# Kernel tuning notes

Measured on AMD Instinct MI355X. Metric: run time of the kernel, lower is better.

The kernel has to match this reference:

```python
import jax, jax.numpy as jnp
import numpy as np

DIM = 1024
HEADS = 16
HD = DIM // HEADS            # 64
MLP = 4 * DIM                # 4096
IN_OUT = MLP + 3 * DIM       # 7168, in_proj out dim
OUT_IN = MLP + DIM           # 5120, out_proj in dim
OUT_OUT = 2 * DIM            # 2048, out_proj out dim
R = 2                        # residual PQ levels
K = 64                       # codebook size
NCB = HEADS                  # num_codebooks = num_heads * codebooks_ratio
IN_CLUSTERS = HEADS * (IN_OUT // DIM)                 # 112
OUT_CLUSTERS = HEADS * max(1, OUT_OUT // OUT_IN)      # 16
SUB_IN = DIM // NCB          # 64
SUB_OUT = OUT_IN // NCB      # 320
EPS = 1e-5


def setup_inputs() -> dict:
    key = jax.random.key(0)
    k1, k2, k3, k4, k5 = jax.random.split(key, 5)
    B, N = 4, 1024
    x = jax.random.normal(k1, (B, N, DIM), jnp.float32)
    in_codebooks = jax.random.normal(k2, (R, IN_CLUSTERS, NCB, K, SUB_IN), jnp.float32) * 0.02
    in_indices = jax.random.randint(k3, (R, IN_OUT, NCB), 0, K, jnp.int32)
    out_codebooks = jax.random.normal(k4, (R, OUT_CLUSTERS, NCB, K, SUB_OUT), jnp.float32) * 0.02
    out_indices = jax.random.randint(k5, (R, OUT_OUT, NCB), 0, K, jnp.int32)
    return {"x": x, "in_codebooks": in_codebooks, "in_indices": in_indices,
            "out_codebooks": out_codebooks, "out_indices": out_indices}


def _decode_weight(cb, idx):
    """Decode RPQ weight. cb: (R, n_clusters, n_codebooks, K, sub), idx: (R, O, n_codebooks).
    Returns dense weight (O, n_codebooks*sub)."""
    Rr, nclust, C, _, sub = cb.shape
    O = idx.shape[1]
    cluster = jnp.arange(O) // (O // nclust)                       # per-row cluster id
    w = cb[jnp.arange(Rr)[:, None, None],
           cluster[None, :, None],
           jnp.arange(C)[None, None, :],
           idx]                                                    # (R, O, C, sub)
    return w.sum(0).reshape(O, C * sub)


def reference(x, in_codebooks, in_indices, out_codebooks, out_indices):
    B, N, C = x.shape
    res = x
    # LayerNorm without affine
    mu = x.mean(-1, keepdims=True)
    var = x.var(-1, keepdims=True)
    xn = (x - mu) * jax.lax.rsqrt(var + EPS)
    # in_proj: dequant + GEMM
    Win = _decode_weight(in_codebooks, in_indices)                 # (IN_OUT, DIM)
    h = jnp.einsum('bnc,oc->bno', xn, Win)                         # (B, N, IN_OUT)
    xm, q, k, v = jnp.split(h, [MLP, MLP + DIM, MLP + 2 * DIM], axis=-1)
    q = q.reshape(B, N, HEADS, HD).transpose(0, 2, 1, 3)
    k = k.reshape(B, N, HEADS, HD).transpose(0, 2, 1, 3)
    v = v.reshape(B, N, HEADS, HD).transpose(0, 2, 1, 3)
    scale = HD ** -0.5
    attn = jax.nn.softmax(jnp.einsum('bhqd,bhkd->bhqk', q, k) * scale, axis=-1)
    xa = jnp.einsum('bhqk,bhkd->bhqd', attn, v).transpose(0, 2, 1, 3).reshape(B, N, C)
    # out_proj: dequant + GEMM on concatenated [mlp, attn]
    Wout = _decode_weight(out_codebooks, out_indices)              # (OUT_OUT, OUT_IN)
    o = jnp.einsum('bnc,oc->bno', jnp.concatenate([xm, xa], axis=-1), Wout)
    x_mlp, x_attn = o[..., :DIM], o[..., DIM:]
    return x_mlp + x_attn + res
```

## Files before the change

kernel.cpp:

```cpp
#include <hip/hip_runtime.h>
#include <hip/hip_bf16.h>

typedef float f32x4 __attribute__((ext_vector_type(4)));
typedef short short8 __attribute__((ext_vector_type(8)));

#define LDH 7168
#define MFMA16(d, x, y) d = __builtin_amdgcn_mfma_f32_16x16x32_bf16(x, y, d, 0, 0, 0)

__device__ __forceinline__ void async_ld16(const void* g, void* l) {
  __builtin_amdgcn_global_load_lds(
      (const __attribute__((address_space(1))) unsigned int*)g,
      (__attribute__((address_space(3))) unsigned int*)l, 16, 0, 0);
}

__device__ __forceinline__ float bf2f(unsigned short u) {
  union { unsigned int i; float f; } c; c.i = ((unsigned int)u) << 16; return c.f;
}

__device__ __forceinline__ ushort4 pack_bf16x4(float4 v) {
  ushort4 u;
  __hip_bfloat16 b;
  b = __float2bfloat16(v.x); u.x = *(unsigned short*)&b;
  b = __float2bfloat16(v.y); u.y = *(unsigned short*)&b;
  b = __float2bfloat16(v.z); u.z = *(unsigned short*)&b;
  b = __float2bfloat16(v.w); u.w = *(unsigned short*)&b;
  return u;
}

__global__ __launch_bounds__(256) void prep_k(const float* __restrict__ x,
                                              const float* __restrict__ in_cb,
                                              const int* __restrict__ in_idx,
                                              const float* __restrict__ out_cb,
                                              const int* __restrict__ out_idx,
                                              __hip_bfloat16* __restrict__ Win,
                                              __hip_bfloat16* __restrict__ Weff,
                                              __hip_bfloat16* __restrict__ xn) {
  const int bid = blockIdx.x;
  if (bid < 7168) {
    const int o = bid;
    const int cluster = o >> 6;
    const int c = threadIdx.x >> 4;
    const int s4 = (threadIdx.x & 15) * 4;
    const int k0 = in_idx[o * 16 + c];
    const int k1 = in_idx[(7168 + o) * 16 + c];
    const float4 v0 = *(const float4*)&in_cb[((((size_t)cluster) * 16 + c) * 64 + k0) * 64 + s4];
    const float4 v1 = *(const float4*)&in_cb[((((size_t)(112 + cluster)) * 16 + c) * 64 + k1) * 64 + s4];
    float4 v; v.x = v0.x + v1.x; v.y = v0.y + v1.y; v.z = v0.z + v1.z; v.w = v0.w + v1.w;
    *(ushort4*)&Win[(size_t)o * 1024 + c * 64 + s4] = pack_bf16x4(v);
  } else if (bid < 8192) {
    const int o = bid - 7168;
    const int cl1 = o >> 7, cl2 = cl1 + 8;
    for (int e4 = threadIdx.x * 4; e4 < 5120; e4 += 1024) {
      const int c = e4 / 320, s = e4 - c * 320;
      float4 acc = {0.f, 0.f, 0.f, 0.f};
      #pragma unroll
      for (int r = 0; r < 2; ++r) {
        const int ka = out_idx[((size_t)r * 2048 + o) * 16 + c];
        const int kb = out_idx[((size_t)r * 2048 + o + 1024) * 16 + c];
        const float4 va = *(const float4*)&out_cb[((((size_t)r * 16 + cl1) * 16 + c) * 64 + ka) * 320 + s];
        const float4 vb = *(const float4*)&out_cb[((((size_t)r * 16 + cl2) * 16 + c) * 64 + kb) * 320 + s];
        acc.x += va.x + vb.x; acc.y += va.y + vb.y; acc.z += va.z + vb.z; acc.w += va.w + vb.w;
      }
      *(ushort4*)&Weff[(size_t)o * 5120 + e4] = pack_bf16x4(acc);
    }
  } else {
    const int row = bid - 8192;
    const float4 v = ((const float4*)(x + (size_t)row * 1024))[threadIdx.x];
    float s = v.x + v.y + v.z + v.w;
    float s2 = v.x * v.x + v.y * v.y + v.z * v.z + v.w * v.w;
    #pragma unroll
    for (int off = 32; off > 0; off >>= 1) {
      s += __shfl_down(s, off, 64);
      s2 += __shfl_down(s2, off, 64);
    }
    __shared__ float red[8];
    if ((threadIdx.x & 63) == 0) { red[threadIdx.x >> 6] = s; red[4 + (threadIdx.x >> 6)] = s2; }
    __syncthreads();
    s = red[0] + red[1] + red[2] + red[3];
    s2 = red[4] + red[5] + red[6] + red[7];
    const float mu = s * (1.f / 1024.f);
    const float rstd = rsqrtf(s2 * (1.f / 1024.f) - mu * mu + 1e-5f);
    float4 nv;
    nv.x = (v.x - mu) * rstd; nv.y = (v.y - mu) * rstd;
    nv.z = (v.z - mu) * rstd; nv.w = (v.w - mu) * rstd;
    *(ushort4*)(xn + (size_t)row * 1024 + threadIdx.x * 4) = pack_bf16x4(nv);
  }
}

__global__ __launch_bounds__(512, 2) void gemm1_k(const __hip_bfloat16* __restrict__ A,
                                                  const __hip_bfloat16* __restrict__ B,
                                                  __hip_bfloat16* __restrict__ C,
                                                  __hip_bfloat16* __restrict__ vT) {
  __shared__ ushort sm[65536];
  const int tid = threadIdx.x;
  const int lane = tid & 63, wid = tid >> 6;
  const int g = lane >> 4, r16 = lane & 15;
  const int wr = wid >> 2, wc = wid & 3;

  const int x = blockIdx.x & 7, local = blockIdx.x >> 3;
  const int mb = (x >> 1) * 4 + local / 14;
  const int nb = (x & 1) * 14 + local % 14;
  const int m0 = mb * 256, n0 = nb * 256;

  auto stageA = [&](int kt, int base) {
    #pragma unroll
    for (int i = 0; i < 4; ++i) {
      const int c = i * 512 + tid;
      const int lc = c ^ (((c >> 5) & 1) << 1);
      const int row = lc >> 3, col = (lc & 7) * 8;
      async_ld16(&A[(size_t)(m0 + row) * 1024 + kt * 64 + col], &sm[base + c * 8]);
    }
  };
  auto stageB = [&](int kt, int base) {
    #pragma unroll
    for (int i = 0; i < 4; ++i) {
      const int c = i * 512 + tid;
      const int lc = c ^ (((c >> 5) & 1) << 1);
      const int row = lc >> 3, col = (lc & 7) * 8;
      async_ld16(&B[(size_t)(n0 + row) * 1024 + kt * 64 + col], &sm[base + 16384 + c * 8]);
    }
  };
  auto rdA = [&](int base, int mm, int kk) -> short8 {
    const int row = wr * 128 + mm * 16 + r16;
    int e = row * 64 + kk * 32 + g * 8;
    e ^= ((row >> 2) & 1) << 4;
    return *(const short8*)&sm[base + e];
  };
  auto rdB = [&](int base, int nn, int kk) -> short8 {
    const int row = wc * 64 + nn * 16 + r16;
    int e = row * 64 + kk * 32 + g * 8;
    e ^= ((row >> 2) & 1) << 4;
    return *(const short8*)&sm[base + 16384 + e];
  };

  f32x4 acc[8][4] = {};

  stageA(0, 0); stageB(0, 0);
  asm volatile("s_waitcnt vmcnt(0)" ::: "memory");
  __builtin_amdgcn_s_barrier();
  __builtin_amdgcn_sched_barrier(0);

  auto tile_body = [&](int kt, int base, int nbase) {
    short8 a0[4][2], a1[4][2], b0[2][2], b1[2][2];
    #pragma unroll
    for (int mm = 0; mm < 4; ++mm) { a0[mm][0] = rdA(base, mm, 0); a0[mm][1] = rdA(base, mm, 1); }
    #pragma unroll
    for (int nn = 0; nn < 2; ++nn) { b0[nn][0] = rdB(base, nn, 0); b0[nn][1] = rdB(base, nn, 1); }
    if (kt + 1 < 16) stageA(kt + 1, nbase);
    __builtin_amdgcn_s_setprio(1);
    #pragma unroll
    for (int mm = 0; mm < 4; ++mm)
      #pragma unroll
      for (int nn = 0; nn < 2; ++nn) {
        MFMA16(acc[mm][nn], a0[mm][0], b0[nn][0]);
        MFMA16(acc[mm][nn], a0[mm][1], b0[nn][1]);
      }
    __builtin_amdgcn_s_setprio(0);
    __builtin_amdgcn_s_barrier();
    #pragma unroll
    for (int nn = 0; nn < 2; ++nn) { b1[nn][0] = rdB(base, 2 + nn, 0); b1[nn][1] = rdB(base, 2 + nn, 1); }
    if (kt + 1 < 16) stageB(kt + 1, nbase);
    __builtin_amdgcn_s_setprio(1);
    #pragma unroll
    for (int mm = 0; mm < 4; ++mm)
      #pragma unroll
      for (int nn = 0; nn < 2; ++nn) {
        MFMA16(acc[mm][2 + nn], a0[mm][0], b1[nn][0]);
        MFMA16(acc[mm][2 + nn], a0[mm][1], b1[nn][1]);
      }
    __builtin_amdgcn_s_setprio(0);
    __builtin_amdgcn_s_barrier();
    #pragma unroll
    for (int mm = 0; mm < 4; ++mm) { a1[mm][0] = rdA(base, 4 + mm, 0); a1[mm][1] = rdA(base, 4 + mm, 1); }
    __builtin_amdgcn_s_setprio(1);
    #pragma unroll
    for (int mm = 0; mm < 4; ++mm)
      #pragma unroll
      for (int nn = 0; nn < 2; ++nn) {
        MFMA16(acc[4 + mm][2 + nn], a1[mm][0], b1[nn][0]);
        MFMA16(acc[4 + mm][2 + nn], a1[mm][1], b1[nn][1]);
      }
    __builtin_amdgcn_s_setprio(0);
    __builtin_amdgcn_s_barrier();
    __builtin_amdgcn_s_setprio(1);
    #pragma unroll
    for (int mm = 0; mm < 4; ++mm)
      #pragma unroll
      for (int nn = 0; nn < 2; ++nn) {
        MFMA16(acc[4 + mm][nn], a1[mm][0], b0[nn][0]);
        MFMA16(acc[4 + mm][nn], a1[mm][1], b0[nn][1]);
      }
    __builtin_amdgcn_s_setprio(0);
    asm volatile("s_waitcnt vmcnt(0) lgkmcnt(0)" ::: "memory");
    __builtin_amdgcn_s_barrier();
    __builtin_amdgcn_sched_barrier(0);
  };

  for (int kt = 0; kt < 16; kt += 2) {
    tile_body(kt, 0, 32768);
    tile_body(kt + 1, 32768, 0);
  }

  if (n0 < 6144) {
    #pragma unroll
    for (int mm = 0; mm < 8; ++mm)
      #pragma unroll
      for (int nn = 0; nn < 4; ++nn)
        #pragma unroll
        for (int r = 0; r < 4; ++r) {
          const int m = m0 + wr * 128 + mm * 16 + g * 4 + r;
          const int o = n0 + wc * 64 + nn * 16 + r16;
          C[(size_t)m * LDH + o] = __float2bfloat16(acc[mm][nn][r]);
        }
  } else {
    #pragma unroll
    for (int mm = 0; mm < 8; ++mm)
      #pragma unroll
      for (int nn = 0; nn < 4; ++nn)
        #pragma unroll
        for (int r = 0; r < 4; ++r) {
          const int m = m0 + wr * 128 + mm * 16 + g * 4 + r;
          const int o = n0 + wc * 64 + nn * 16 + r16;
          const int b_ = m >> 10;
          vT[((size_t)b_ * 1024 + (o - 6144)) * 1024 + (m & 1023)] = __float2bfloat16(acc[mm][nn][r]);
        }
  }
}

__global__ __launch_bounds__(256) void attn_k(const __hip_bfloat16* __restrict__ h,
                                              const __hip_bfloat16* __restrict__ vT,
                                              __hip_bfloat16* __restrict__ po0,
                                              __hip_bfloat16* __restrict__ po1,
                                              __hip_bfloat16* __restrict__ po2,
                                              __hip_bfloat16* __restrict__ po3,
                                              float* __restrict__ lbuf) {
  const int qt = blockIdx.x & 15, kvs = blockIdx.x >> 4;
  const int head = blockIdx.y, b = blockIdx.z;
  const int tid = threadIdx.x;
  const int lane = tid & 63, w = tid >> 6;
  const int g = lane >> 4, r16 = lane & 15;

  __shared__ __align__(16) __hip_bfloat16 Ks[2][64 * 64];
  __shared__ __align__(16) __hip_bfloat16 Vs[2][64 * 64];
  __shared__ __align__(16) __hip_bfloat16 P[4][16][72];

  const __hip_bfloat16* Kg = h + (size_t)(b * 1024) * LDH + 5120 + head * 64;
  const __hip_bfloat16* Vg = vT + ((size_t)b * 1024 + head * 64) * 1024;

  const size_t qrow = (size_t)(b * 1024 + qt * 64 + w * 16 + r16);
  short8 aq0 = *(const short8*)&h[qrow * LDH + 4096 + head * 64 + g * 8];
  short8 aq1 = *(const short8*)&h[qrow * LDH + 4096 + head * 64 + 32 + g * 8];

  auto stage = [&](int buf, int t) {
    #pragma unroll
    for (int i = 0; i < 2; ++i) {
      const int c_lin = i * 256 + tid;
      const int row = c_lin >> 3;
      const int c_log = (c_lin & 7) ^ (row & 7);
      async_ld16(&Kg[(size_t)(t * 64 + row) * LDH + c_log * 8], &Ks[buf][c_lin * 8]);
    }
    #pragma unroll
    for (int i = 0; i < 2; ++i) {
      const int c_lin = i * 256 + tid;
      const int row = c_lin >> 3;
      const int c_log = (c_lin & 7) ^ (row & 7);
      async_ld16(&Vg[(size_t)row * 1024 + t * 64 + c_log * 8], &Vs[buf][c_lin * 8]);
    }
  };

  f32x4 o_acc[4] = {};
  float l_r[4] = {0.f, 0.f, 0.f, 0.f};

  const int t0 = kvs * 4;
  stage(0, t0);
  for (int tt = 0; tt < 4; ++tt) {
    const int buf = tt & 1;
    if (tt + 1 < 4) {
      stage(buf ^ 1, t0 + tt + 1);
      asm volatile("s_waitcnt vmcnt(4)" ::: "memory");
    } else {
      asm volatile("s_waitcnt vmcnt(0)" ::: "memory");
    }
    __builtin_amdgcn_s_barrier();
    __builtin_amdgcn_sched_barrier(0);

    f32x4 s_acc[4] = {};
    #pragma unroll
    for (int nn = 0; nn < 4; ++nn) {
      const int row = nn * 16 + r16;
      short8 bk0 = *(const short8*)&Ks[buf][row * 64 + ((g ^ (row & 7)) * 8)];
      short8 bk1 = *(const short8*)&Ks[buf][row * 64 + (((g + 4) ^ (row & 7)) * 8)];
      s_acc[nn] = __builtin_amdgcn_mfma_f32_16x16x32_bf16(aq0, bk0, s_acc[nn], 0, 0, 0);
      s_acc[nn] = __builtin_amdgcn_mfma_f32_16x16x32_bf16(aq1, bk1, s_acc[nn], 0, 0, 0);
    }

    #pragma unroll
    for (int nn = 0; nn < 4; ++nn)
      #pragma unroll
      for (int r = 0; r < 4; ++r) {
        const float p = __expf(s_acc[nn][r] * 0.125f);
        s_acc[nn][r] = p;
        l_r[r] += p;
      }

    #pragma unroll
    for (int nn = 0; nn < 4; ++nn)
      #pragma unroll
      for (int r = 0; r < 4; ++r)
        P[w][g * 4 + r][nn * 16 + r16] = __float2bfloat16(s_acc[nn][r]);
    short8 ap0 = *(const short8*)&P[w][r16][g * 8];
    short8 ap1 = *(const short8*)&P[w][r16][32 + g * 8];

    #pragma unroll
    for (int nn = 0; nn < 4; ++nn) {
      const int row = nn * 16 + r16;
      short8 bv0 = *(const short8*)&Vs[buf][row * 64 + ((g ^ (row & 7)) * 8)];
      short8 bv1 = *(const short8*)&Vs[buf][row * 64 + (((g + 4) ^ (row & 7)) * 8)];
      o_acc[nn] = __builtin_amdgcn_mfma_f32_16x16x32_bf16(ap0, bv0, o_acc[nn], 0, 0, 0);
      o_acc[nn] = __builtin_amdgcn_mfma_f32_16x16x32_bf16(ap1, bv1, o_acc[nn], 0, 0, 0);
    }
    __builtin_amdgcn_s_barrier();
    __builtin_amdgcn_sched_barrier(0);
  }

  __hip_bfloat16* po = (kvs == 0) ? po0 : (kvs == 1) ? po1 : (kvs == 2) ? po2 : po3;
  #pragma unroll
  for (int r = 0; r < 4; ++r) {
    float l = l_r[r];
    #pragma unroll
    for (int off = 1; off < 16; off <<= 1) l += __shfl_xor(l, off, 64);
    const size_t mrow = (size_t)(b * 1024 + qt * 64 + w * 16 + g * 4 + r);
    #pragma unroll
    for (int nn = 0; nn < 4; ++nn)
      po[mrow * 1024 + head * 64 + nn * 16 + r16] = __float2bfloat16(o_acc[nn][r]);
    if (r16 == 0) lbuf[(mrow * 16 + head) * 4 + kvs] = l;
  }
}

__global__ __launch_bounds__(256) void combine_k(const __hip_bfloat16* __restrict__ po0,
                                                 const __hip_bfloat16* __restrict__ po2,
                                                 const __hip_bfloat16* __restrict__ po3,
                                                 const float* __restrict__ lbuf,
                                                 __hip_bfloat16* __restrict__ xa) {
  const int row = blockIdx.x;
  const int e4 = threadIdx.x * 4;
  const int head = e4 >> 6;
  const float* lb = &lbuf[(((size_t)row) * 16 + head) * 4];
  const float inv = 1.0f / (lb[0] + lb[1] + lb[2] + lb[3]);
  const ushort4 a = *(const ushort4*)&po0[(size_t)row * 1024 + e4];
  const ushort4 bb = *(const ushort4*)&xa[(size_t)row * 1024 + e4];
  const ushort4 c = *(const ushort4*)&po2[(size_t)row * 1024 + e4];
  const ushort4 d = *(const ushort4*)&po3[(size_t)row * 1024 + e4];
  float4 v;
  v.x = (bf2f(a.x) + bf2f(bb.x) + bf2f(c.x) + bf2f(d.x)) * inv;
  v.y = (bf2f(a.y) + bf2f(bb.y) + bf2f(c.y) + bf2f(d.y)) * inv;
  v.z = (bf2f(a.z) + bf2f(bb.z) + bf2f(c.z) + bf2f(d.z)) * inv;
  v.w = (bf2f(a.w) + bf2f(bb.w) + bf2f(c.w) + bf2f(d.w)) * inv;
  *(ushort4*)&xa[(size_t)row * 1024 + e4] = pack_bf16x4(v);
}

__global__ __launch_bounds__(512, 2) void gemm2_k(const __hip_bfloat16* __restrict__ h,
                                                  const __hip_bfloat16* __restrict__ xa,
                                                  const __hip_bfloat16* __restrict__ W,
                                                  __hip_bfloat16* __restrict__ p0,
                                                  __hip_bfloat16* __restrict__ p1,
                                                  __hip_bfloat16* __restrict__ p2,
                                                  float* __restrict__ out) {
  __shared__ ushort sm[65536];
  const int tid = threadIdx.x;
  const int lane = tid & 63, wid = tid >> 6;
  const int g = lane >> 4, r16 = lane & 15;
  const int wr = wid >> 2, wc = wid & 3;

  int bid = blockIdx.x;
  bid = (bid & 7) * 8 + (bid >> 3);
  const int mb = bid >> 2, nb = bid & 3;
  const int m0 = mb * 256, n0 = nb * 256;
  const int z = blockIdx.y;
  const int kt0 = z * 20, ktEnd = kt0 + 20;

  auto stageA = [&](int kt, int base) {
    const __hip_bfloat16* Ab; size_t lda; int kc;
    if (kt < 64) { Ab = h;  lda = LDH;  kc = kt * 64; }
    else         { Ab = xa; lda = 1024; kc = kt * 64 - 4096; }
    #pragma unroll
    for (int i = 0; i < 4; ++i) {
      const int c = i * 512 + tid;
      const int lc = c ^ (((c >> 5) & 1) << 1);
      const int row = lc >> 3, col = (lc & 7) * 8;
      async_ld16(&Ab[(size_t)(m0 + row) * lda + kc + col], &sm[base + c * 8]);
    }
  };
  auto stageB = [&](int kt, int base) {
    #pragma unroll
    for (int i = 0; i < 4; ++i) {
      const int c = i * 512 + tid;
      const int lc = c ^ (((c >> 5) & 1) << 1);
      const int row = lc >> 3, col = (lc & 7) * 8;
      async_ld16(&W[(size_t)(n0 + row) * 5120 + kt * 64 + col], &sm[base + 16384 + c * 8]);
    }
  };
  auto rdA = [&](int base, int mm, int kk) -> short8 {
    const int row = wr * 128 + mm * 16 + r16;
    int e = row * 64 + kk * 32 + g * 8;
    e ^= ((row >> 2) & 1) << 4;
    return *(const short8*)&sm[base + e];
  };
  auto rdB = [&](int base, int nn, int kk) -> short8 {
    const int row = wc * 64 + nn * 16 + r16;
    int e = row * 64 + kk * 32 + g * 8;
    e ^= ((row >> 2) & 1) << 4;
    return *(const short8*)&sm[base + 16384 + e];
  };

  f32x4 acc[8][4] = {};

  stageA(kt0, 0); stageB(kt0, 0);
  asm volatile("s_waitcnt vmcnt(0)" ::: "memory");
  __builtin_amdgcn_s_barrier();
  __builtin_amdgcn_sched_barrier(0);

  auto tile_body = [&](int kt, int base, int nbase) {
    short8 a0[4][2], a1[4][2], b0[2][2], b1[2][2];
    #pragma unroll
    for (int mm = 0; mm < 4; ++mm) { a0[mm][0] = rdA(base, mm, 0); a0[mm][1] = rdA(base, mm, 1); }
    #pragma unroll
    for (int nn = 0; nn < 2; ++nn) { b0[nn][0] = rdB(base, nn, 0); b0[nn][1] = rdB(base, nn, 1); }
    if (kt + 1 < ktEnd) stageA(kt + 1, nbase);
    __builtin_amdgcn_s_setprio(1);
    #pragma unroll
    for (int mm = 0; mm < 4; ++mm)
      #pragma unroll
      for (int nn = 0; nn < 2; ++nn) {
        MFMA16(acc[mm][nn], a0[mm][0], b0[nn][0]);
        MFMA16(acc[mm][nn], a0[mm][1], b0[nn][1]);
      }
    __builtin_amdgcn_s_setprio(0);
    __builtin_amdgcn_s_barrier();
    #pragma unroll
    for (int nn = 0; nn < 2; ++nn) { b1[nn][0] = rdB(base, 2 + nn, 0); b1[nn][1] = rdB(base, 2 + nn, 1); }
    if (kt + 1 < ktEnd) stageB(kt + 1, nbase);
    __builtin_amdgcn_s_setprio(1);
    #pragma unroll
    for (int mm = 0; mm < 4; ++mm)
      #pragma unroll
      for (int nn = 0; nn < 2; ++nn) {
        MFMA16(acc[mm][2 + nn], a0[mm][0], b1[nn][0]);
        MFMA16(acc[mm][2 + nn], a0[mm][1], b1[nn][1]);
      }
    __builtin_amdgcn_s_setprio(0);
    __builtin_amdgcn_s_barrier();
    #pragma unroll
    for (int mm = 0; mm < 4; ++mm) { a1[mm][0] = rdA(base, 4 + mm, 0); a1[mm][1] = rdA(base, 4 + mm, 1); }
    __builtin_amdgcn_s_setprio(1);
    #pragma unroll
    for (int mm = 0; mm < 4; ++mm)
      #pragma unroll
      for (int nn = 0; nn < 2; ++nn) {
        MFMA16(acc[4 + mm][2 + nn], a1[mm][0], b1[nn][0]);
        MFMA16(acc[4 + mm][2 + nn], a1[mm][1], b1[nn][1]);
      }
    __builtin_amdgcn_s_setprio(0);
    __builtin_amdgcn_s_barrier();
    __builtin_amdgcn_s_setprio(1);
    #pragma unroll
    for (int mm = 0; mm < 4; ++mm)
      #pragma unroll
      for (int nn = 0; nn < 2; ++nn) {
        MFMA16(acc[4 + mm][nn], a1[mm][0], b0[nn][0]);
        MFMA16(acc[4 + mm][nn], a1[mm][1], b0[nn][1]);
      }
    __builtin_amdgcn_s_setprio(0);
    asm volatile("s_waitcnt vmcnt(0) lgkmcnt(0)" ::: "memory");
    __builtin_amdgcn_s_barrier();
    __builtin_amdgcn_sched_barrier(0);
  };

  for (int kt = kt0; kt < ktEnd; kt += 2) {
    tile_body(kt, 0, 32768);
    tile_body(kt + 1, 32768, 0);
  }

  __hip_bfloat16* pz = (z == 0) ? p0 : (z == 1) ? p1 : p2;
  #pragma unroll
  for (int mm = 0; mm < 8; ++mm)
    #pragma unroll
    for (int nn = 0; nn < 4; ++nn)
      #pragma unroll
      for (int r = 0; r < 4; ++r) {
        const int m = m0 + wr * 128 + mm * 16 + g * 4 + r;
        const int n = n0 + wc * 64 + nn * 16 + r16;
        if (z == 3) out[(size_t)m * 1024 + n] = acc[mm][nn][r];
        else        pz[(size_t)m * 1024 + n] = __float2bfloat16(acc[mm][nn][r]);
      }
}

__global__ __launch_bounds__(256) void reduce_k(const __hip_bfloat16* __restrict__ p0,
                                                const __hip_bfloat16* __restrict__ p1,
                                                const __hip_bfloat16* __restrict__ p2,
                                                const float* __restrict__ res,
                                                float* __restrict__ out) {
  const size_t i4 = (size_t)blockIdx.x * 256 + threadIdx.x;
  float4 o = ((const float4*)out)[i4];
  const float4 rr = ((const float4*)res)[i4];
  const ushort4 a0 = ((const ushort4*)p0)[i4];
  const ushort4 a1 = ((const ushort4*)p1)[i4];
  const ushort4 a2 = ((const ushort4*)p2)[i4];
  o.x += rr.x + bf2f(a0.x) + bf2f(a1.x) + bf2f(a2.x);
  o.y += rr.y + bf2f(a0.y) + bf2f(a1.y) + bf2f(a2.y);
  o.z += rr.z + bf2f(a0.z) + bf2f(a1.z) + bf2f(a2.z);
  o.w += rr.w + bf2f(a0.w) + bf2f(a1.w) + bf2f(a2.w);
  ((float4*)out)[i4] = o;
}

extern "C" void kernel_launch(void* const* d_in, const int* in_sizes, int n_in,
                              void* d_out, int out_size, void* d_ws, size_t ws_size,
                              hipStream_t stream) {
  (void)in_sizes; (void)n_in; (void)out_size; (void)ws_size;
  const float* x      = (const float*)d_in[0];
  const float* in_cb  = (const float*)d_in[1];
  const int*   in_idx = (const int*)d_in[2];
  const float* out_cb = (const float*)d_in[3];
  const int*   out_idx= (const int*)d_in[4];
  float* out = (float*)d_out;
  char* ws = (char*)d_ws;

  __hip_bfloat16* Win  = (__hip_bfloat16*)(ws);
  __hip_bfloat16* Weff = (__hip_bfloat16*)(ws + 14680064);
  __hip_bfloat16* xn   = (__hip_bfloat16*)(ws + 25165824);
  __hip_bfloat16* h    = (__hip_bfloat16*)(ws + 33554432);
  __hip_bfloat16* vT   = (__hip_bfloat16*)(ws + 92274688);
  __hip_bfloat16* xa   = (__hip_bfloat16*)(ws + 100663296);

  __hip_bfloat16* po0  = Win;
  __hip_bfloat16* po2  = (__hip_bfloat16*)out;
  __hip_bfloat16* po3  = (__hip_bfloat16*)out + 4194304;
  float*          lbuf = (float*)xn;
  __hip_bfloat16* pk0 = Win;
  __hip_bfloat16* pk1 = xn;
  __hip_bfloat16* pk2 = vT;

  prep_k<<<dim3(12288), dim3(256), 0, stream>>>(x, in_cb, in_idx, out_cb, out_idx, Win, Weff, xn);
  gemm1_k<<<dim3(448), dim3(512), 0, stream>>>(xn, Win, h, vT);
  attn_k<<<dim3(64, 16, 4), dim3(256), 0, stream>>>(h, vT, po0, xa, po2, po3, lbuf);
  combine_k<<<dim3(4096), dim3(256), 0, stream>>>(po0, po2, po3, lbuf, xa);
  gemm2_k<<<dim3(64, 4), dim3(512), 0, stream>>>(h, xa, Weff, pk0, pk1, pk2, out);
  reduce_k<<<dim3(4096), dim3(256), 0, stream>>>(pk0, pk1, pk2, x, out);
}
```

Before: 203.4 us.

## Replace split-K reduce kernel with atomic adds and halve attention KV splits

The residual copy into the output moves into the prep kernel, and the split-K partial outputs of gemm2 are accumulated into the fp32 output with atomicAdd. This removes the separate reduce kernel and its bf16 partial buffers. Attention now uses 2 KV splits instead of 4, each processing 8 tiles, which shrinks combine work and partial traffic but halves the attention grid. Atomic accumulation makes summation order nondeterministic and adds atomic traffic.

New measurement: 231.1 us. 1.14x slower.

```diff
diff --git a/kernel.cpp b/kernel.cpp
--- a/kernel.cpp
+++ b/kernel.cpp
@@ -34,7 +34,8 @@
                                               const int* __restrict__ out_idx,
                                               __hip_bfloat16* __restrict__ Win,
                                               __hip_bfloat16* __restrict__ Weff,
-                                              __hip_bfloat16* __restrict__ xn) {
+                                              __hip_bfloat16* __restrict__ xn,
+                                              float* __restrict__ out) {
   const int bid = blockIdx.x;
   if (bid < 7168) {
     const int o = bid;
@@ -63,7 +64,7 @@
       }
       *(ushort4*)&Weff[(size_t)o * 5120 + e4] = pack_bf16x4(acc);
     }
-  } else {
+  } else if (bid < 12288) {
     const int row = bid - 8192;
     const float4 v = ((const float4*)(x + (size_t)row * 1024))[threadIdx.x];
     float s = v.x + v.y + v.z + v.w;
@@ -84,6 +85,10 @@
     nv.x = (v.x - mu) * rstd; nv.y = (v.y - mu) * rstd;
     nv.z = (v.z - mu) * rstd; nv.w = (v.w - mu) * rstd;
     *(ushort4*)(xn + (size_t)row * 1024 + threadIdx.x * 4) = pack_bf16x4(nv);
+  } else {
+    const int row = bid - 12288;
+    const size_t i4 = (size_t)row * 256 + threadIdx.x;
+    ((float4*)out)[i4] = ((const float4*)x)[i4];
   }
 }
 
@@ -231,8 +236,6 @@
                                               const __hip_bfloat16* __restrict__ vT,
                                               __hip_bfloat16* __restrict__ po0,
                                               __hip_bfloat16* __restrict__ po1,
-                                              __hip_bfloat16* __restrict__ po2,
-                                              __hip_bfloat16* __restrict__ po3,
                                               float* __restrict__ lbuf) {
   const int qt = blockIdx.x & 15, kvs = blockIdx.x >> 4;
   const int head = blockIdx.y, b = blockIdx.z;
@@ -271,11 +274,11 @@
   f32x4 o_acc[4] = {};
   float l_r[4] = {0.f, 0.f, 0.f, 0.f};
 
-  const int t0 = kvs * 4;
+  const int t0 = kvs * 8;
   stage(0, t0);
-  for (int tt = 0; tt < 4; ++tt) {
+  for (int tt = 0; tt < 8; ++tt) {
     const int buf = tt & 1;
-    if (tt + 1 < 4) {
+    if (tt + 1 < 8) {
       stage(buf ^ 1, t0 + tt + 1);
       asm volatile("s_waitcnt vmcnt(4)" ::: "memory");
     } else {
@@ -323,7 +326,7 @@
     __builtin_amdgcn_sched_barrier(0);
   }
 
-  __hip_bfloat16* po = (kvs == 0) ? po0 : (kvs == 1) ? po1 : (kvs == 2) ? po2 : po3;
+  __hip_bfloat16* po = kvs ? po1 : po0;
   #pragma unroll
   for (int r = 0; r < 4; ++r) {
     float l = l_r[r];
@@ -333,38 +336,32 @@
     #pragma unroll
     for (int nn = 0; nn < 4; ++nn)
       po[mrow * 1024 + head * 64 + nn * 16 + r16] = __float2bfloat16(o_acc[nn][r]);
-    if (r16 == 0) lbuf[(mrow * 16 + head) * 4 + kvs] = l;
+    if (r16 == 0) lbuf[(mrow * 16 + head) * 2 + kvs] = l;
   }
 }
 
 __global__ __launch_bounds__(256) void combine_k(const __hip_bfloat16* __restrict__ po0,
-                                                 const __hip_bfloat16* __restrict__ po2,
-                                                 const __hip_bfloat16* __restrict__ po3,
                                                  const float* __restrict__ lbuf,
                                                  __hip_bfloat16* __restrict__ xa) {
   const int row = blockIdx.x;
   const int e4 = threadIdx.x * 4;
   const int head = e4 >> 6;
-  const float* lb = &lbuf[(((size_t)row) * 16 + head) * 4];
-  const float inv = 1.0f / (lb[0] + lb[1] + lb[2] + lb[3]);
+  const float l = lbuf[(((size_t)row) * 16 + head) * 2 + 0]
+                + lbuf[(((size_t)row) * 16 + head) * 2 + 1];
+  const float inv = 1.0f / l;
   const ushort4 a = *(const ushort4*)&po0[(size_t)row * 1024 + e4];
   const ushort4 bb = *(const ushort4*)&xa[(size_t)row * 1024 + e4];
-  const ushort4 c = *(const ushort4*)&po2[(size_t)row * 1024 + e4];
-  const ushort4 d = *(const ushort4*)&po3[(size_t)row * 1024 + e4];
   float4 v;
-  v.x = (bf2f(a.x) + bf2f(bb.x) + bf2f(c.x) + bf2f(d.x)) * inv;
-  v.y = (bf2f(a.y) + bf2f(bb.y) + bf2f(c.y) + bf2f(d.y)) * inv;
-  v.z = (bf2f(a.z) + bf2f(bb.z) + bf2f(c.z) + bf2f(d.z)) * inv;
-  v.w = (bf2f(a.w) + bf2f(bb.w) + bf2f(c.w) + bf2f(d.w)) * inv;
+  v.x = (bf2f(a.x) + bf2f(bb.x)) * inv;
+  v.y = (bf2f(a.y) + bf2f(bb.y)) * inv;
+  v.z = (bf2f(a.z) + bf2f(bb.z)) * inv;
+  v.w = (bf2f(a.w) + bf2f(bb.w)) * inv;
   *(ushort4*)&xa[(size_t)row * 1024 + e4] = pack_bf16x4(v);
 }
 
 __global__ __launch_bounds__(512, 2) void gemm2_k(const __hip_bfloat16* __restrict__ h,
                                                   const __hip_bfloat16* __restrict__ xa,
                                                   const __hip_bfloat16* __restrict__ W,
-                                                  __hip_bfloat16* __restrict__ p0,
-                                                  __hip_bfloat16* __restrict__ p1,
-                                                  __hip_bfloat16* __restrict__ p2,
                                                   float* __restrict__ out) {
   __shared__ ushort sm[65536];
   const int tid = threadIdx.x;
@@ -481,7 +478,6 @@
     tile_body(kt + 1, 32768, 0);
   }
 
-  __hip_bfloat16* pz = (z == 0) ? p0 : (z == 1) ? p1 : p2;
   #pragma unroll
   for (int mm = 0; mm < 8; ++mm)
     #pragma unroll
@@ -490,27 +486,8 @@
       for (int r = 0; r < 4; ++r) {
         const int m = m0 + wr * 128 + mm * 16 + g * 4 + r;
         const int n = n0 + wc * 64 + nn * 16 + r16;
-        if (z == 3) out[(size_t)m * 1024 + n] = acc[mm][nn][r];
-        else        pz[(size_t)m * 1024 + n] = __float2bfloat16(acc[mm][nn][r]);
-      }
-}
-
-__global__ __launch_bounds__(256) void reduce_k(const __hip_bfloat16* __restrict__ p0,
-                                                const __hip_bfloat16* __restrict__ p1,
-                                                const __hip_bfloat16* __restrict__ p2,
-                                                const float* __restrict__ res,
-                                                float* __restrict__ out) {
-  const size_t i4 = (size_t)blockIdx.x * 256 + threadIdx.x;
-  float4 o = ((const float4*)out)[i4];
-  const float4 rr = ((const float4*)res)[i4];
-  const ushort4 a0 = ((const ushort4*)p0)[i4];
-  const ushort4 a1 = ((const ushort4*)p1)[i4];
-  const ushort4 a2 = ((const ushort4*)p2)[i4];
-  o.x += rr.x + bf2f(a0.x) + bf2f(a1.x) + bf2f(a2.x);
-  o.y += rr.y + bf2f(a0.y) + bf2f(a1.y) + bf2f(a2.y);
-  o.z += rr.z + bf2f(a0.z) + bf2f(a1.z) + bf2f(a2.z);
-  o.w += rr.w + bf2f(a0.w) + bf2f(a1.w) + bf2f(a2.w);
-  ((float4*)out)[i4] = o;
+        atomicAdd(&out[(size_t)m * 1024 + n], acc[mm][nn][r]);
+      }
 }
 
 extern "C" void kernel_launch(void* const* d_in, const int* in_sizes, int n_in,
@@ -533,17 +510,11 @@
   __hip_bfloat16* xa   = (__hip_bfloat16*)(ws + 100663296);
 
   __hip_bfloat16* po0  = Win;
-  __hip_bfloat16* po2  = (__hip_bfloat16*)out;
-  __hip_bfloat16* po3  = (__hip_bfloat16*)out + 4194304;
   float*          lbuf = (float*)xn;
-  __hip_bfloat16* pk0 = Win;
-  __hip_bfloat16* pk1 = xn;
-  __hip_bfloat16* pk2 = vT;
-
-  prep_k<<<dim3(12288), dim3(256), 0, stream>>>(x, in_cb, in_idx, out_cb, out_idx, Win, Weff, xn);
+
+  prep_k<<<dim3(16384), dim3(256), 0, stream>>>(x, in_cb, in_idx, out_cb, out_idx, Win, Weff, xn, out);
   gemm1_k<<<dim3(448), dim3(512), 0, stream>>>(xn, Win, h, vT);
-  attn_k<<<dim3(64, 16, 4), dim3(256), 0, stream>>>(h, vT, po0, xa, po2, po3, lbuf);
-  combine_k<<<dim3(4096), dim3(256), 0, stream>>>(po0, po2, po3, lbuf, xa);
-  gemm2_k<<<dim3(64, 4), dim3(512), 0, stream>>>(h, xa, Weff, pk0, pk1, pk2, out);
-  reduce_k<<<dim3(4096), dim3(256), 0, stream>>>(pk0, pk1, pk2, x, out);
-}
+  attn_k<<<dim3(32, 16, 4), dim3(256), 0, stream>>>(h, vT, po0, xa, lbuf);
+  combine_k<<<dim3(4096), dim3(256), 0, stream>>>(po0, lbuf, xa);
+  gemm2_k<<<dim3(64, 4), dim3(512), 0, stream>>>(h, xa, Weff, out);
+}
```
